# Performance work log

Hardware: AMD Instinct MI355X
Metric: run time of the kernel (lower is better)

The kernel has to match this reference:

```python
import jax, jax.numpy as jnp
import numpy as np

N_FEAT = 64
N_PROJ = 32
N_OUT = 128
LN_EPS = 1e-5


def setup_inputs() -> dict:
    key = jax.random.key(0)
    ks = jax.random.split(key, 8)
    n_seq, n_res = 256, 384
    M = jax.random.normal(ks[0], (1, n_seq, n_res, N_FEAT), dtype=jnp.float32)
    M_mask = jnp.ones((1, n_seq, n_res), dtype=jnp.float32)
    Z_raw = jax.random.normal(ks[1], (1, n_res, n_res, N_OUT), dtype=jnp.float32)
    s = 1.0 / np.sqrt(N_FEAT)
    Wa = jax.random.uniform(ks[2], (N_PROJ, N_FEAT), jnp.float32, -s, s)
    ba = jnp.zeros((N_PROJ,), jnp.float32)
    Wb = jax.random.uniform(ks[3], (N_PROJ, N_FEAT), jnp.float32, -s, s)
    bb = jnp.zeros((N_PROJ,), jnp.float32)
    so = 1.0 / np.sqrt(N_PROJ * N_PROJ)
    Wo = jax.random.uniform(ks[4], (N_OUT, N_PROJ * N_PROJ), jnp.float32, -so, so)
    bo = jnp.zeros((N_OUT,), jnp.float32)
    gamma = jnp.ones((N_FEAT,), jnp.float32)
    beta = jnp.zeros((N_FEAT,), jnp.float32)
    return {"M": M, "M_mask": M_mask, "Z_raw": Z_raw, "gamma": gamma, "beta": beta,
            "Wa": Wa, "ba": ba, "Wb": Wb, "bb": bb, "Wo": Wo, "bo": bo}


def reference(M, M_mask, Z_raw, gamma, beta, Wa, ba, Wb, bb, Wo, bo):
    # LayerNorm over last dim
    mu = jnp.mean(M, axis=-1, keepdims=True)
    var = jnp.mean(jnp.square(M - mu), axis=-1, keepdims=True)
    Mn = (M - mu) * jax.lax.rsqrt(var + LN_EPS) * gamma + beta
    # projections [1, s, r, p]
    left = jnp.einsum('bsrf,pf->bsrp', Mn, Wa) + ba
    right = jnp.einsum('bsrf,pf->bsrp', Mn, Wb) + bb
    mask = M_mask[..., None]  # [1, s, r, 1]
    left = mask * left
    right = mask * right
    # norm[i,j] = sum_s mask[s,i]*mask[s,j]
    norm = jnp.einsum('sa,sd->ad', M_mask[0], M_mask[0])[None, :, :, None]
    n_res, p = left.shape[2], left.shape[3]
    # outer-product mean: O[i,j,c,d] = sum_s left[s,i,c] * right[s,j,d]
    O = jnp.einsum('sic,sjd->ijcd', left[0], right[0])
    O = O.reshape(n_res, n_res, p * p)
    Z = jnp.einsum('ijk,ok->ijo', O, Wo) + bo  # [r, r, n_out]
    Z = Z[None] / (0.001 + norm)
    return Z + Z_raw
```

## Files before the change

### kernel.cpp

```cpp
#include <hip/hip_runtime.h>

typedef unsigned short u16;
typedef u16   u16x4 __attribute__((ext_vector_type(4)));
typedef u16   u16x8 __attribute__((ext_vector_type(8)));
typedef short s16x8 __attribute__((ext_vector_type(8)));
typedef float f32x4 __attribute__((ext_vector_type(4)));

#define NSEQ 256
#define NRES 384
#define NF   64
#define NP   32
#define NO   128

__device__ __forceinline__ u16 f2b(float f) {
    union { float f; unsigned u; } c; c.f = f;
    unsigned r = c.u + 0x7fffu + ((c.u >> 16) & 1u);
    return (u16)(r >> 16);
}
__device__ __forceinline__ float b2f(u16 h) {
    union { unsigned u; float f; } c; c.u = ((unsigned)h) << 16;
    return c.f;
}

__device__ __forceinline__ void gload_lds16(const u16* g, u16* l) {
    __builtin_amdgcn_global_load_lds(
        (const __attribute__((address_space(1))) unsigned int*)(g),
        (__attribute__((address_space(3))) unsigned int*)(l),
        16, 0, 0);
}

__global__ __launch_bounds__(256) void k_pre(
    const float* __restrict__ M, const float* __restrict__ mask,
    const float* __restrict__ gamma, const float* __restrict__ beta,
    const float* __restrict__ Wa, const float* __restrict__ ba,
    const float* __restrict__ Wb, const float* __restrict__ bb,
    const float* __restrict__ Wo,
    u16* __restrict__ leftT, u16* __restrict__ rightT,
    float* __restrict__ normMat, u16* __restrict__ WoB)
{
    __shared__ __align__(16) char sm[52480];
    const int b = blockIdx.x, t = threadIdx.x;

    if (b < 768) {
        const int sC = b / 24, iC = b % 24;
        const int i0 = iC * 16, s0 = sC * 8;

        u16*   hiP   = (u16*)sm;
        u16*   loP   = (u16*)sm + 8192;
        u16*   WP    = (u16*)(sm + 32768);
        float* mkP   = (float*)(sm + 51200);
        float* biasP = (float*)(sm + 51712);
        float* glP   = (float*)(sm + 51968);
        float* blP   = (float*)(sm + 52224);

        const int wv = t >> 6, ln = t & 63;
        const int quad = ln >> 4, l16 = ln & 15;

        {
            const int rl = ln >> 4, c = ln & 15;
            #pragma unroll
            for (int q = 0; q < 8; ++q) {
                int rbase = wv * 32 + q * 4;
                int r   = rbase + rl;
                int xsw = (r & 3) << 1;
                const float* src = M + ((long)(s0 + (r & 7)) * NRES + (i0 + (r >> 3))) * NF
                                     + ((c ^ xsw) << 2);
                gload_lds16((const u16*)src, (u16*)sm + rbase * 128);
            }
        }
        {
            const int side = t >> 7, p = (t >> 2) & 31, qq = t & 3;
            const float* Wg = (side ? Wb : Wa) + p * 64 + qq * 16;
            u16x8 h[2], l[2];
            #pragma unroll
            for (int u = 0; u < 4; ++u) {
                f32x4 w4 = *(const f32x4*)(Wg + u * 4);
                #pragma unroll
                for (int e = 0; e < 4; ++e) {
                    u16 hb = f2b(w4[e]);
                    h[u >> 1][(u & 1) * 4 + e] = hb;
                    l[u >> 1][(u & 1) * 4 + e] = f2b(w4[e] - b2f(hb));
                }
            }
            int hbase = ((side * 2 + 0) * 32 + p) * 72 + qq * 16;
            int lbase = ((side * 2 + 1) * 32 + p) * 72 + qq * 16;
            *(u16x8*)(WP + hbase)     = h[0];
            *(u16x8*)(WP + hbase + 8) = h[1];
            *(u16x8*)(WP + lbase)     = l[0];
            *(u16x8*)(WP + lbase + 8) = l[1];
        }
        if (t < 128) mkP[t] = mask[(long)(s0 + (t & 7)) * NRES + i0 + (t >> 3)];
        if (t < 64) { glP[t] = gamma[t]; blP[t] = beta[t];
                      biasP[t] = (t < 32) ? ba[t] : bb[t - 32]; }
        __syncthreads();

        const int r = t >> 1, half = t & 1;
        const int xsw = (r & 3) << 1, psw = r & 3;
        f32x4 v[8];
        {
            const float* raw = (const float*)sm + r * 64;
            #pragma unroll
            for (int e = 0; e < 8; ++e)
                v[e] = *(const f32x4*)(raw + (((half * 8 + e) ^ xsw) << 2));
        }
        float sum = 0.f, sq = 0.f;
        #pragma unroll
        for (int e = 0; e < 8; ++e)
            #pragma unroll
            for (int j = 0; j < 4; ++j) { float x = v[e][j]; sum += x; sq += x * x; }
        sum += __shfl_xor(sum, 1); sq += __shfl_xor(sq, 1);
        float mu  = sum * (1.f / 64.f);
        float var = sq * (1.f / 64.f) - mu * mu;
        float rs  = rsqrtf(var + 1e-5f);
        #pragma unroll
        for (int e = 0; e < 8; ++e) {
            int og = half * 8 + e;
            f32x4 g4 = *(const f32x4*)(glP + og * 4);
            f32x4 b4 = *(const f32x4*)(blP + og * 4);
            #pragma unroll
            for (int j = 0; j < 4; ++j) v[e][j] = (v[e][j] - mu) * rs * g4[j] + b4[j];
        }
        __syncthreads();

        #pragma unroll
        for (int d = 0; d < 4; ++d) {
            u16x8 h8, l8;
            #pragma unroll
            for (int j = 0; j < 4; ++j) {
                u16 hb = f2b(v[2 * d][j]);
                h8[j] = hb; l8[j] = f2b(v[2 * d][j] - b2f(hb));
                u16 hb2 = f2b(v[2 * d + 1][j]);
                h8[4 + j] = hb2; l8[4 + j] = f2b(v[2 * d + 1][j] - b2f(hb2));
            }
            int q = (half * 4 + d) ^ psw;
            *(u16x8*)(hiP + r * 64 + q * 8) = h8;
            *(u16x8*)(loP + r * 64 + q * 8) = l8;
        }
        __syncthreads();

        const int wbase = wv * 32;
        f32x4 acc[2][4] = {};
        #pragma unroll
        for (int k = 0; k < 2; ++k) {
            u16x8 ah[2], al[2];
            #pragma unroll
            for (int rt = 0; rt < 2; ++rt) {
                int row = wbase + rt * 16 + l16;
                int gk  = (quad + k * 4) ^ (row & 3);
                ah[rt] = *(const u16x8*)(hiP + row * 64 + gk * 8);
                al[rt] = *(const u16x8*)(loP + row * 64 + gk * 8);
            }
            #pragma unroll
            for (int pt = 0; pt < 4; ++pt) {
                int side = pt >> 1, ph = pt & 1;
                int hrow = ((side * 2 + 0) * 32 + ph * 16 + l16) * 72 + (quad + k * 4) * 8;
                int lrow = ((side * 2 + 1) * 32 + ph * 16 + l16) * 72 + (quad + k * 4) * 8;
                u16x8 bh = *(const u16x8*)(WP + hrow);
                u16x8 bl = *(const u16x8*)(WP + lrow);
                #pragma unroll
                for (int rt = 0; rt < 2; ++rt) {
                    acc[rt][pt] = __builtin_amdgcn_mfma_f32_16x16x32_bf16(
                        (s16x8)ah[rt], (s16x8)bh, acc[rt][pt], 0, 0, 0);
                    acc[rt][pt] = __builtin_amdgcn_mfma_f32_16x16x32_bf16(
                        (s16x8)al[rt], (s16x8)bh, acc[rt][pt], 0, 0, 0);
                    acc[rt][pt] = __builtin_amdgcn_mfma_f32_16x16x32_bf16(
                        (s16x8)ah[rt], (s16x8)bl, acc[rt][pt], 0, 0, 0);
                }
            }
        }

        #pragma unroll
        for (int rt = 0; rt < 2; ++rt) {
            int rowb = wbase + rt * 16 + quad * 4;
            f32x4 mk4 = *(const f32x4*)(mkP + rowb);
            int ii = rowb >> 3, sb = rowb & 7;
            #pragma unroll
            for (int pt = 0; pt < 4; ++pt) {
                int side = pt >> 1, p = (pt & 1) * 16 + l16;
                float bv = biasP[side * 32 + p];
                u16x4 ov;
                #pragma unroll
                for (int rg = 0; rg < 4; ++rg)
                    ov[rg] = f2b((acc[rt][pt][rg] + bv) * mk4[rg]);
                u16* dst = (side ? rightT : leftT)
                         + ((long)(i0 + ii) * NP + p) * NSEQ + s0 + sb;
                *(u16x4*)dst = ov;
            }
        }

    } else if (b < 896) {
        int idx = (b - 768) * 256 + t;
        int o   = idx >> 8;
        int kp  = (idx & 255) << 2;
        int l16 = (kp >> 2) & 15;
        int ntb = (kp >> 6) & 1;
        int qd  = (kp >> 7) & 3;
        int mtb = (kp >> 9) & 1;
        const float* src = Wo + o * 1024 + (mtb * 16 + qd * 4) * 32 + ntb * 16 + l16;
        u16x4 w;
        #pragma unroll
        for (int rg = 0; rg < 4; ++rg) w[rg] = f2b(src[rg * 32]);
        *(u16x4*)(WoB + o * 1024 + kp) = w;

    } else {
        float (*mi)[17] = (float (*)[17])sm;
        float (*mj)[17] = (float (*)[17])(sm + 17408);
        const int bn = b - 896;
        const int iB = (bn / 24) * 16, jB = (bn % 24) * 16;
        #pragma unroll
        for (int it = 0; it < 16; ++it) {
            int ss = it * 16 + (t >> 4);
            int c  = t & 15;
            mi[ss][c] = mask[(long)ss * NRES + iB + c];
            mj[ss][c] = mask[(long)ss * NRES + jB + c];
        }
        __syncthreads();
        const int ti = t >> 4, tj = t & 15;
        float acc = 0.f;
        for (int ss = 0; ss < 256; ++ss) acc += mi[ss][ti] * mj[ss][tj];
        normMat[(long)(iB + ti) * NRES + jB + tj] = acc;
    }
}

__global__ __launch_bounds__(512, 4) void k_main(
    const u16* __restrict__ leftT, const u16* __restrict__ rightT,
    const float* __restrict__ normMat,
    const u16* __restrict__ WoB, const float* __restrict__ bo,
    const float* __restrict__ Zraw, float* __restrict__ out)
{
    __shared__ __align__(16) u16 smem[36864];

    const int t    = threadIdx.x;
    const int wave = t >> 6, lane = t & 63;
    const int quad = lane >> 4, l16 = lane & 15;
    const int wr = wave >> 1, wc = wave & 1;

    const int bid = blockIdx.x;
    const int r_  = bid >> 3;
    const int bx  = r_ / 12;
    const int by  = (bid & 7) * 12 + (r_ % 12);
    const int icBase = bx * 256;
    const int jdBase = by * 128;

    const int srow = lane >> 2;
    const int g8   = ((lane & 3) ^ ((srow >> 1) & 3)) * 8;

    f32x4 acc[4][4] = {};

    const u16* aSrc0 = leftT  + (icBase + wave * 32 + srow) * NSEQ + g8;
    const u16* aSrc1 = aSrc0 + 16 * NSEQ;
    const u16* bSrc  = rightT + (jdBase + wave * 16 + srow) * NSEQ + g8;

    #define STAGE(bb, k0) do {                                                   \
        gload_lds16(aSrc0 + (k0), &smem[(bb) * 12288 + wave * 1024]);            \
        gload_lds16(aSrc1 + (k0), &smem[(bb) * 12288 + wave * 1024 + 512]);      \
        gload_lds16(bSrc  + (k0), &smem[(bb) * 12288 + 8192 + wave * 512]);      \
    } while (0)

    STAGE(0, 0);
    STAGE(1, 32);

    #pragma unroll
    for (int kt = 0; kt < 8; ++kt) {
        if (kt < 7) asm volatile("s_waitcnt vmcnt(3)" ::: "memory");
        else        asm volatile("s_waitcnt vmcnt(0)" ::: "memory");
        __builtin_amdgcn_s_barrier();
        __builtin_amdgcn_sched_barrier(0);
        if (kt < 6) STAGE((kt + 2) % 3, (kt + 2) * 32);

        const int bb = kt % 3;
        const int gx = (quad ^ ((l16 >> 1) & 3)) * 8;
        u16x8 af[4], bf[4];
        const u16* Ab = &smem[bb * 12288 + (wr * 64 + l16) * 32 + gx];
        const u16* Bb = &smem[bb * 12288 + 8192 + (wc * 64 + l16) * 32 + gx];
        #pragma unroll
        for (int mt = 0; mt < 4; ++mt) af[mt] = *(const u16x8*)(Ab + mt * 512);
        #pragma unroll
        for (int nt = 0; nt < 4; ++nt) bf[nt] = *(const u16x8*)(Bb + nt * 512);

        __builtin_amdgcn_s_setprio(1);
        #pragma unroll
        for (int mt = 0; mt < 4; ++mt)
            #pragma unroll
            for (int nt = 0; nt < 4; ++nt)
                acc[mt][nt] = __builtin_amdgcn_mfma_f32_16x16x32_bf16(
                    (s16x8)af[mt], (s16x8)bf[nt], acc[mt][nt], 0, 0, 0);
        __builtin_amdgcn_s_setprio(0);
    }
    #undef STAGE
    __syncthreads();

    #pragma unroll
    for (int mt = 0; mt < 4; ++mt) {
        #pragma unroll
        for (int nt = 0; nt < 4; ++nt) {
            int pair = (wr * 2 + (mt >> 1)) * 4 + wc * 2 + (nt >> 1);
            int kp   = l16 * 4 + (nt & 1) * 64 + quad * 128 + (mt & 1) * 512;
            int ks   = kp ^ (quad << 4) ^ ((pair & 7) << 3);
            u16x4 wv;
            #pragma unroll
            for (int rg = 0; rg < 4; ++rg) wv[rg] = f2b(acc[mt][nt][rg]);
            *(u16x4*)&smem[pair * 1024 + ks] = wv;
        }
    }
    __syncthreads();

    f32x4 acc2[2][2] = {};
    const int oh = wave & 3, kh = wave >> 2;
    const int ob = oh * 32;
    const int pxor = (l16 & 7) << 3;
    const u16* wp0 = WoB + (long)(ob + l16) * 1024 + kh * 512 + quad * 8;
    const u16* wp1 = wp0 + 16 * 1024;
    const u16* os0 = &smem[l16 * 1024];
    const u16* os1 = &smem[(16 + l16) * 1024];
    #pragma unroll 8
    for (int kk = 0; kk < 16; ++kk) {
        int kp = kh * 512 + kk * 32 + quad * 8;
        int ks = kp ^ (((kp >> 7) & 3) << 4) ^ pxor;
        u16x8 a0 = *(const u16x8*)(os0 + ks);
        u16x8 a1 = *(const u16x8*)(os1 + ks);
        u16x8 b0 = *(const u16x8*)(wp0 + kk * 32);
        u16x8 b1 = *(const u16x8*)(wp1 + kk * 32);
        __builtin_amdgcn_s_setprio(1);
        acc2[0][0] = __builtin_amdgcn_mfma_f32_16x16x32_bf16((s16x8)a0, (s16x8)b0, acc2[0][0], 0, 0, 0);
        acc2[0][1] = __builtin_amdgcn_mfma_f32_16x16x32_bf16((s16x8)a0, (s16x8)b1, acc2[0][1], 0, 0, 0);
        acc2[1][0] = __builtin_amdgcn_mfma_f32_16x16x32_bf16((s16x8)a1, (s16x8)b0, acc2[1][0], 0, 0, 0);
        acc2[1][1] = __builtin_amdgcn_mfma_f32_16x16x32_bf16((s16x8)a1, (s16x8)b1, acc2[1][1], 0, 0, 0);
        __builtin_amdgcn_s_setprio(0);
    }
    __syncthreads();

    float* zs = (float*)smem;
    if (kh == 0) {
        #pragma unroll
        for (int ph = 0; ph < 2; ++ph)
            #pragma unroll
            for (int n2 = 0; n2 < 2; ++n2)
                #pragma unroll
                for (int rg = 0; rg < 4; ++rg)
                    zs[(ph * 16 + quad * 4 + rg) * 132 + ob + n2 * 16 + l16]
                        = acc2[ph][n2][rg];
    }
    __syncthreads();
    if (kh == 1) {
        #pragma unroll
        for (int ph = 0; ph < 2; ++ph)
            #pragma unroll
            for (int n2 = 0; n2 < 2; ++n2)
                #pragma unroll
                for (int rg = 0; rg < 4; ++rg)
                    zs[(ph * 16 + quad * 4 + rg) * 132 + ob + n2 * 16 + l16]
                        += acc2[ph][n2][rg];
    }
    __syncthreads();

    const int i0 = bx * 8, j0 = by * 4;
    const int pr = t >> 4, o0 = (t & 15) * 8;
    const int i = i0 + (pr >> 2), j = j0 + (pr & 3);
    const float rn = 1.f / (0.001f + normMat[i * NRES + j]);
    const long base = ((long)(i * NRES + j)) * NO + o0;
    f32x4 z0  = *(const f32x4*)&zs[pr * 132 + o0];
    f32x4 z1  = *(const f32x4*)&zs[pr * 132 + o0 + 4];
    f32x4 zr0 = *(const f32x4*)(Zraw + base);
    f32x4 zr1 = *(const f32x4*)(Zraw + base + 4);
    f32x4 bv0 = *(const f32x4*)(bo + o0);
    f32x4 bv1 = *(const f32x4*)(bo + o0 + 4);
    f32x4 r0, r1;
    #pragma unroll
    for (int e = 0; e < 4; ++e) r0[e] = (z0[e] + bv0[e]) * rn + zr0[e];
    #pragma unroll
    for (int e = 0; e < 4; ++e) r1[e] = (z1[e] + bv1[e]) * rn + zr1[e];
    *(f32x4*)(out + base)     = r0;
    *(f32x4*)(out + base + 4) = r1;
}

extern "C" void kernel_launch(void* const* d_in, const int* in_sizes, int n_in,
                              void* d_out, int out_size, void* d_ws, size_t ws_size,
                              hipStream_t stream)
{
    const float* M     = (const float*)d_in[0];
    const float* mask  = (const float*)d_in[1];
    const float* Zraw  = (const float*)d_in[2];
    const float* gamma = (const float*)d_in[3];
    const float* beta  = (const float*)d_in[4];
    const float* Wa    = (const float*)d_in[5];
    const float* ba    = (const float*)d_in[6];
    const float* Wb    = (const float*)d_in[7];
    const float* bb    = (const float*)d_in[8];
    const float* Wo    = (const float*)d_in[9];
    const float* bo    = (const float*)d_in[10];
    float* out = (float*)d_out;

    char* ws = (char*)d_ws;
    u16*   leftT   = (u16*)ws;
    u16*   rightT  = (u16*)(ws + 6291456);
    float* normMat = (float*)(ws + 12582912);
    u16*   WoB     = (u16*)(ws + 13172736);

    k_pre<<<dim3(1472), dim3(256), 0, stream>>>(M, mask, gamma, beta,
                                                Wa, ba, Wb, bb, Wo,
                                                leftT, rightT, normMat, WoB);
    k_main<<<dim3(4608), dim3(512), 0, stream>>>(leftT, rightT, normMat,
                                                 WoB, bo, Zraw, out);
}
```

Baseline: 342.9 us.

## Prefetch Wo-GEMM operands and split-K reduce via dual LDS buffers

Software-pipelines the final Wo GEMM loop by loading the next iteration's LDS and global operands before issuing the current MFMAs, and drops the setprio hints. The split-K reduction now has both wave halves write to separate LDS regions in one step instead of a store, barrier, read-modify-write sequence, removing one barrier. Zraw, norm and bias loads are hoisted ahead of the barrier so their global latency overlaps the reduction. This raises register pressure and needs the second LDS region to fit within the existing shared buffer.

After: 354.6 us. +3.4%, slower.

```diff
diff --git a/kernel.cpp b/kernel.cpp
--- a/kernel.cpp
+++ b/kernel.cpp
@@ -313,63 +313,65 @@
     const u16* wp1 = wp0 + 16 * 1024;
     const u16* os0 = &smem[l16 * 1024];
     const u16* os1 = &smem[(16 + l16) * 1024];
-    #pragma unroll 8
+
+    int kp_ = kh * 512 + quad * 8;
+    int ks_ = kp_ ^ (((kp_ >> 7) & 3) << 4) ^ pxor;
+    u16x8 pa0 = *(const u16x8*)(os0 + ks_);
+    u16x8 pa1 = *(const u16x8*)(os1 + ks_);
+    u16x8 pb0 = *(const u16x8*)(wp0);
+    u16x8 pb1 = *(const u16x8*)(wp1);
+    #pragma unroll
     for (int kk = 0; kk < 16; ++kk) {
-        int kp = kh * 512 + kk * 32 + quad * 8;
-        int ks = kp ^ (((kp >> 7) & 3) << 4) ^ pxor;
-        u16x8 a0 = *(const u16x8*)(os0 + ks);
-        u16x8 a1 = *(const u16x8*)(os1 + ks);
-        u16x8 b0 = *(const u16x8*)(wp0 + kk * 32);
-        u16x8 b1 = *(const u16x8*)(wp1 + kk * 32);
-        __builtin_amdgcn_s_setprio(1);
+        u16x8 a0 = pa0, a1 = pa1, b0 = pb0, b1 = pb1;
+        if (kk < 15) {
+            int kp = kh * 512 + (kk + 1) * 32 + quad * 8;
+            int ks = kp ^ (((kp >> 7) & 3) << 4) ^ pxor;
+            pa0 = *(const u16x8*)(os0 + ks);
+            pa1 = *(const u16x8*)(os1 + ks);
+            pb0 = *(const u16x8*)(wp0 + (kk + 1) * 32);
+            pb1 = *(const u16x8*)(wp1 + (kk + 1) * 32);
+        }
         acc2[0][0] = __builtin_amdgcn_mfma_f32_16x16x32_bf16((s16x8)a0, (s16x8)b0, acc2[0][0], 0, 0, 0);
         acc2[0][1] = __builtin_amdgcn_mfma_f32_16x16x32_bf16((s16x8)a0, (s16x8)b1, acc2[0][1], 0, 0, 0);
         acc2[1][0] = __builtin_amdgcn_mfma_f32_16x16x32_bf16((s16x8)a1, (s16x8)b0, acc2[1][0], 0, 0, 0);
         acc2[1][1] = __builtin_amdgcn_mfma_f32_16x16x32_bf16((s16x8)a1, (s16x8)b1, acc2[1][1], 0, 0, 0);
-        __builtin_amdgcn_s_setprio(0);
     }
-    __syncthreads();
-
-    float* zs = (float*)smem;
-    if (kh == 0) {
-        #pragma unroll
-        for (int ph = 0; ph < 2; ++ph)
-            #pragma unroll
-            for (int n2 = 0; n2 < 2; ++n2)
-                #pragma unroll
-                for (int rg = 0; rg < 4; ++rg)
-                    zs[(ph * 16 + quad * 4 + rg) * 132 + ob + n2 * 16 + l16]
-                        = acc2[ph][n2][rg];
-    }
-    __syncthreads();
-    if (kh == 1) {
-        #pragma unroll
-        for (int ph = 0; ph < 2; ++ph)
-            #pragma unroll
-            for (int n2 = 0; n2 < 2; ++n2)
-                #pragma unroll
-                for (int rg = 0; rg < 4; ++rg)
-                    zs[(ph * 16 + quad * 4 + rg) * 132 + ob + n2 * 16 + l16]
-                        += acc2[ph][n2][rg];
-    }
-    __syncthreads();
 
     const int i0 = bx * 8, j0 = by * 4;
     const int pr = t >> 4, o0 = (t & 15) * 8;
     const int i = i0 + (pr >> 2), j = j0 + (pr & 3);
-    const float rn = 1.f / (0.001f + normMat[i * NRES + j]);
     const long base = ((long)(i * NRES + j)) * NO + o0;
-    f32x4 z0  = *(const f32x4*)&zs[pr * 132 + o0];
-    f32x4 z1  = *(const f32x4*)&zs[pr * 132 + o0 + 4];
     f32x4 zr0 = *(const f32x4*)(Zraw + base);
     f32x4 zr1 = *(const f32x4*)(Zraw + base + 4);
+    const float nrmv = normMat[i * NRES + j];
     f32x4 bv0 = *(const f32x4*)(bo + o0);
     f32x4 bv1 = *(const f32x4*)(bo + o0 + 4);
+
+    __syncthreads();
+
+    float* zs0 = (float*)smem;
+    float* zs1 = (float*)((char*)smem + 16896);
+    float* zsw = kh ? zs1 : zs0;
+    #pragma unroll
+    for (int ph = 0; ph < 2; ++ph)
+        #pragma unroll
+        for (int n2 = 0; n2 < 2; ++n2)
+            #pragma unroll
+            for (int rg = 0; rg < 4; ++rg)
+                zsw[(ph * 16 + quad * 4 + rg) * 132 + ob + n2 * 16 + l16]
+                    = acc2[ph][n2][rg];
+    __syncthreads();
+
+    const float rn = 1.f / (0.001f + nrmv);
+    f32x4 za0 = *(const f32x4*)&zs0[pr * 132 + o0];
+    f32x4 za1 = *(const f32x4*)&zs0[pr * 132 + o0 + 4];
+    f32x4 zb0 = *(const f32x4*)&zs1[pr * 132 + o0];
+    f32x4 zb1 = *(const f32x4*)&zs1[pr * 132 + o0 + 4];
     f32x4 r0, r1;
     #pragma unroll
-    for (int e = 0; e < 4; ++e) r0[e] = (z0[e] + bv0[e]) * rn + zr0[e];
-    #pragma unroll
-    for (int e = 0; e < 4; ++e) r1[e] = (z1[e] + bv1[e]) * rn + zr1[e];
+    for (int e = 0; e < 4; ++e) r0[e] = (za0[e] + zb0[e] + bv0[e]) * rn + zr0[e];
+    #pragma unroll
+    for (int e = 0; e < 4; ++e) r1[e] = (za1[e] + zb1[e] + bv1[e]) * rn + zr1[e];
     *(f32x4*)(out + base)     = r0;
     *(f32x4*)(out + base + 4) = r1;
 }
```
